# Optimization experiments

Measured on AMD Instinct MI355X. Metric: run time of the kernel, lower is better.

The kernel has to match this reference:

```python
import jax, jax.numpy as jnp
import numpy as np

B, S, D, H, DM = 2, 2048, 1024, 16, 4
HD = D // H  # head_dim = 64
EPS = 1e-5


def setup_inputs() -> dict:
    key = jax.random.key(0)
    ks = jax.random.split(key, 8)
    s = 0.02
    return {
        "x": jax.random.normal(ks[0], (B, S, D), jnp.float32),
        "wq": jax.random.normal(ks[1], (D, D), jnp.float32) * s,
        "wk": jax.random.normal(ks[2], (D, D), jnp.float32) * s,
        "wv": jax.random.normal(ks[3], (D, D), jnp.float32) * s,
        "wo": jax.random.normal(ks[4], (D, D), jnp.float32) * s,
        "bo": jnp.zeros((D,), jnp.float32),
        "ln1_scale": jnp.ones((D,), jnp.float32),
        "ln1_shift": jnp.zeros((D,), jnp.float32),
        "ln2_scale": jnp.ones((D,), jnp.float32),
        "ln2_shift": jnp.zeros((D,), jnp.float32),
        "w1": jax.random.normal(ks[5], (DM * D, D), jnp.float32) * s,
        "b1": jnp.zeros((DM * D,), jnp.float32),
        "w2": jax.random.normal(ks[6], (D, DM * D), jnp.float32) * s,
        "b2": jnp.zeros((D,), jnp.float32),
    }


def _layernorm(x, scale, shift):
    mean = jnp.mean(x, axis=-1, keepdims=True)
    var = jnp.var(x, axis=-1, keepdims=True)  # unbiased=False
    return scale * (x - mean) * jax.lax.rsqrt(var + EPS) + shift


def _attn(x, wq, wk, wv, wo, bo):
    b, n, d = x.shape
    # torch Linear: y = x @ W.T
    q = (x @ wq.T).reshape(b, n, H, HD).transpose(0, 2, 1, 3)  # [b,h,n,hd]
    k = (x @ wk.T).reshape(b, n, H, HD).transpose(0, 2, 1, 3)
    v = (x @ wv.T).reshape(b, n, H, HD).transpose(0, 2, 1, 3)
    scores = jnp.einsum("bhqd,bhkd->bhqk", q, k)
    causal = jnp.tril(jnp.ones((n, n), bool))
    scores = jnp.where(causal, scores, -jnp.inf)
    w = jax.nn.softmax(scores / np.sqrt(HD).astype(np.float32), axis=-1)
    ctx = jnp.einsum("bhqk,bhkd->bhqd", w, v)
    ctx = ctx.transpose(0, 2, 1, 3).reshape(b, n, d)
    return ctx @ wo.T + bo


def reference(x, wq, wk, wv, wo, bo, ln1_scale, ln1_shift, ln2_scale, ln2_shift, w1, b1, w2, b2):
    h = x + _attn(_layernorm(x, ln1_scale, ln1_shift), wq, wk, wv, wo, bo)
    y = _layernorm(h, ln2_scale, ln2_shift)
    y = jax.nn.relu(y @ w1.T + b1) @ w2.T + b2
    return h + y
```

## Files before the change

kernel.cpp:

```cpp
#include <hip/hip_runtime.h>
#include <hip/hip_bf16.h>

#define DEV __device__ __forceinline__

typedef __attribute__((ext_vector_type(8))) short bf8;
typedef __attribute__((ext_vector_type(4))) float f4;
typedef __attribute__((ext_vector_type(16))) float f16x;

DEV unsigned short f2bf(float f) {
  union { __hip_bfloat16 h; unsigned short u; } c;
  c.h = __float2bfloat16(f);
  return c.u;
}
DEV unsigned int pk2(float a, float b) {
  union { __hip_bfloat162 h; unsigned int u; } c;
  c.h = __hip_bfloat162(__float2bfloat16(a), __float2bfloat16(b));
  return c.u;
}

DEV int2 swz_tile(int ob, int nxt, int nyt) {
  const int nb = nxt * nyt;
  const int cpx = nb >> 3;
  const int W = (ob & 7) * cpx + (ob >> 3);
  const int scw = 4 * nyt;
  const int sc = W / scw, rem = W - sc * scw;
  return make_int2(rem >> 2, sc * 4 + (rem & 3));
}

template<bool BIAS, bool RELU, bool OUTBF, bool WRVT>
__global__ __launch_bounds__(512, 2) void gemm_bt256(
    const unsigned short* __restrict__ A, const unsigned short* __restrict__ B,
    const float* __restrict__ bias, void* __restrict__ Cout,
    int M, int N, int K, int ldc, unsigned short* __restrict__ vtout, int nyt)
{
  __shared__ unsigned short Sl[2][2][256 * 64];
  const int t = threadIdx.x;
  const int w = t >> 6, l = t & 63;
  const int wr = w >> 2, wc = w & 3;
  int2 tt = swz_tile((int)blockIdx.x, N >> 8, nyt);
  const int m0 = tt.x * 256, n0 = tt.y * 256;

  const int srow = w * 32 + (l >> 3);
  const int scol = 8 * ((l & 7) ^ (l >> 3));
  const unsigned short* Ab = A + (size_t)(m0 + srow) * K + scol;
  const unsigned short* Bb = B + (size_t)(n0 + srow) * K + scol;
  const int sdst = w * 2048 + l * 8;

  auto STAGE = [&](int slot, int kt) {
#pragma unroll
    for (int i = 0; i < 4; ++i) {
      __builtin_amdgcn_global_load_lds(
          (const __attribute__((address_space(1))) void*)(Ab + (size_t)i * 8 * K + kt * 64),
          (__attribute__((address_space(3))) void*)(&Sl[slot][0][sdst + i * 512]), 16, 0, 0);
      __builtin_amdgcn_global_load_lds(
          (const __attribute__((address_space(1))) void*)(Bb + (size_t)i * 8 * K + kt * 64),
          (__attribute__((address_space(3))) void*)(&Sl[slot][1][sdst + i * 512]), 16, 0, 0);
    }
  };

  const f4 fz = {0.f, 0.f, 0.f, 0.f};
  f4 acc[8][4];
#pragma unroll
  for (int i = 0; i < 8; ++i)
#pragma unroll
    for (int j = 0; j < 4; ++j) acc[i][j] = fz;

  const int NT = K >> 6;
  STAGE(0, 0);
  __syncthreads();

  for (int T = 0; T < NT; ++T) {
    if (T + 1 < NT) STAGE((T + 1) & 1, T + 1);
    const int sl = T & 1;
#pragma unroll
    for (int ks = 0; ks < 2; ++ks) {
      const int cb = (ks * 64 + ((l >> 4) * 16)) ^ ((l & 7) << 4);
      bf8 af[8], bg[4];
#pragma unroll
      for (int m = 0; m < 8; ++m)
        af[m] = *(const bf8*)((const char*)&Sl[sl][0][(wr * 128 + m * 16 + (l & 15)) * 64] + cb);
#pragma unroll
      for (int n = 0; n < 4; ++n)
        bg[n] = *(const bf8*)((const char*)&Sl[sl][1][(wc * 64 + n * 16 + (l & 15)) * 64] + cb);
      __builtin_amdgcn_s_setprio(1);
#pragma unroll
      for (int m = 0; m < 8; ++m)
#pragma unroll
        for (int n = 0; n < 4; ++n)
          acc[m][n] = __builtin_amdgcn_mfma_f32_16x16x32_bf16(af[m], bg[n], acc[m][n], 0, 0, 0);
      __builtin_amdgcn_s_setprio(0);
    }
    __syncthreads();
  }

#pragma unroll
  for (int n = 0; n < 4; ++n) {
    const int col = n0 + wc * 64 + n * 16 + (l & 15);
    float bv = 0.f;
    if (BIAS) bv = bias[col];
    const bool isv = WRVT && (col >= 2048);
    const int hh = (col - 2048) >> 6, dd = (col - 2048) & 63;
#pragma unroll
    for (int m = 0; m < 8; ++m) {
#pragma unroll
      for (int r = 0; r < 4; ++r) {
        const int row = m0 + wr * 128 + m * 16 + ((l >> 4) * 4) + r;
        float v = acc[m][n][r] + bv;
        if (RELU) v = fmaxf(v, 0.f);
        if (WRVT && isv) {
          const int bb = row >> 11, ss = row & 2047;
          vtout[((size_t)(bb * 16 + hh) * 64 + dd) * 2048 + ss] = f2bf(v);
        } else if (OUTBF) {
          ((unsigned short*)Cout)[(size_t)row * ldc + col] = f2bf(v);
        } else {
          ((float*)Cout)[(size_t)row * ldc + col] = v;
        }
      }
    }
  }
}

template<bool BIAS, bool RELU, bool RESID, bool OUTBF>
__global__ __launch_bounds__(256) void gemm_bt(
    const unsigned short* __restrict__ A, const unsigned short* __restrict__ B,
    const float* __restrict__ bias, const float* __restrict__ resid,
    void* __restrict__ Cout, int M, int N, int K, int ldc, int nyt)
{
  __shared__ unsigned short Al[2][128 * 32];
  __shared__ unsigned short Bl[2][128 * 32];
  const int t = threadIdx.x;
  const int w = t >> 6, l = t & 63;
  const int wr = w >> 1, wc = w & 1;
  int2 tt = swz_tile((int)blockIdx.x, N >> 7, nyt);
  const int m0 = tt.x * 128, n0 = tt.y * 128;

  const int srow = w * 16 + (l >> 2);
  const int scsw = ((l & 3) * 8) ^ (((srow >> 1) & 3) << 3);
  const unsigned short* Ab = A + (size_t)(m0 + srow) * K + scsw;
  const unsigned short* Bb = B + (size_t)(n0 + srow) * K + scsw;
  const int sdst = w * 512 + l * 8;

  auto STAGE = [&](int slot, int k0) {
#pragma unroll
    for (int i = 0; i < 2; ++i) {
      __builtin_amdgcn_global_load_lds(
          (const __attribute__((address_space(1))) void*)(Ab + (size_t)i * 64 * K + k0),
          (__attribute__((address_space(3))) void*)(&Al[slot][sdst + i * 2048]), 16, 0, 0);
      __builtin_amdgcn_global_load_lds(
          (const __attribute__((address_space(1))) void*)(Bb + (size_t)i * 64 * K + k0),
          (__attribute__((address_space(3))) void*)(&Bl[slot][sdst + i * 2048]), 16, 0, 0);
    }
  };

  const f4 fz = {0.f, 0.f, 0.f, 0.f};
  f4 acc[4][4];
#pragma unroll
  for (int i = 0; i < 4; ++i)
#pragma unroll
    for (int j = 0; j < 4; ++j) acc[i][j] = fz;

  const int NT = K >> 5;
  STAGE(0, 0);
  __syncthreads();

  for (int T = 0; T < NT; ++T) {
    if (T + 1 < NT) STAGE((T + 1) & 1, (T + 1) * 32);
    const int sl = T & 1;
    const int rdcol = ((l >> 4) * 8) ^ ((((l & 15) >> 1) & 3) << 3);
    bf8 af[4], bg[4];
#pragma unroll
    for (int am = 0; am < 4; ++am)
      af[am] = *(const bf8*)&Al[sl][(wr * 64 + am * 16 + (l & 15)) * 32 + rdcol];
#pragma unroll
    for (int bn = 0; bn < 4; ++bn)
      bg[bn] = *(const bf8*)&Bl[sl][(wc * 64 + bn * 16 + (l & 15)) * 32 + rdcol];
    __builtin_amdgcn_s_setprio(1);
#pragma unroll
    for (int am = 0; am < 4; ++am)
#pragma unroll
      for (int bn = 0; bn < 4; ++bn)
        acc[am][bn] = __builtin_amdgcn_mfma_f32_16x16x32_bf16(af[am], bg[bn], acc[am][bn], 0, 0, 0);
    __builtin_amdgcn_s_setprio(0);
    __syncthreads();
  }

#pragma unroll
  for (int bn = 0; bn < 4; ++bn) {
    const int col = n0 + wc * 64 + bn * 16 + (l & 15);
    float bv = 0.f;
    if (BIAS) bv = bias[col];
#pragma unroll
    for (int am = 0; am < 4; ++am) {
#pragma unroll
      for (int r = 0; r < 4; ++r) {
        const int row = m0 + wr * 64 + am * 16 + ((l >> 4) * 4) + r;
        float v = acc[am][bn][r] + bv;
        if (RELU) v = fmaxf(v, 0.f);
        if (RESID) v += resid[(size_t)row * ldc + col];
        if (OUTBF) ((unsigned short*)Cout)[(size_t)row * ldc + col] = f2bf(v);
        else       ((float*)Cout)[(size_t)row * ldc + col] = v;
      }
    }
  }
}

__global__ __launch_bounds__(128) void attn_kernel(
    const unsigned short* __restrict__ qk, const unsigned short* __restrict__ vt,
    unsigned short* __restrict__ ctx)
{
  __shared__ unsigned short Ks[2][64 * 64];
  __shared__ unsigned short Vs[2][64 * 64];

  const int t = threadIdx.x;
  const int w = t >> 6, l = t & 63;
  const int hi = l >> 5, q = l & 31;
  const int bid = blockIdx.x;
  const int xcd = bid & 7, i = bid >> 3;
  const int g = i >> 5, c = i & 31;
  const int a = (g & 1) ? c : 31 - c;
  const int bh = xcd * 4 + g;
  const int b = bh >> 4, h = bh & 15;
  const int tile = 2 * a + w;
  const int q0w = tile * 32;
  const int nit = a + 1;

  const unsigned short* qbase = qk + ((size_t)b * 2048) * 2048 + h * 64;
  const unsigned short* kbase = qbase + 1024;
  const unsigned short* vbase = vt + (size_t)bh * 64 * 2048;

  bf8 qf[4];
#pragma unroll
  for (int ksl = 0; ksl < 4; ++ksl)
    qf[ksl] = *(const bf8*)(qbase + (size_t)(q0w + q) * 2048 + ksl * 16 + hi * 8);

  f16x oacc[2];
#pragma unroll
  for (int dn = 0; dn < 2; ++dn)
#pragma unroll
    for (int i2 = 0; i2 < 16; ++i2) oacc[dn][i2] = 0.f;
  float m_ = -1e30f, l_ = 0.f;

  auto STAGE = [&](int buf, int it) {
#pragma unroll
    for (int s = 0; s < 4; ++s) {
      const int row = s * 16 + (t >> 3);
      const int cb = (t & 7) * 16;
      const int sb = cb ^ ((row & 7) << 4);
      __builtin_amdgcn_global_load_lds(
          (const __attribute__((address_space(1))) void*)
              (kbase + (size_t)(it * 64 + row) * 2048 + (sb >> 1)),
          (__attribute__((address_space(3))) void*)(&Ks[buf][row * 64 + (cb >> 1)]),
          16, 0, 0);
      __builtin_amdgcn_global_load_lds(
          (const __attribute__((address_space(1))) void*)
              (vbase + (size_t)row * 2048 + it * 64 + (sb >> 1)),
          (__attribute__((address_space(3))) void*)(&Vs[buf][row * 64 + (cb >> 1)]),
          16, 0, 0);
    }
  };

  STAGE(0, 0);
  __syncthreads();

  for (int it = 0; it < nit; ++it) {
    const int buf = it & 1;
    if (it + 1 < nit) STAGE(buf ^ 1, it + 1);
    const int kb0 = it * 64;

    f16x s0, s1;
#pragma unroll
    for (int i2 = 0; i2 < 16; ++i2) { s0[i2] = 0.f; s1[i2] = 0.f; }
    __builtin_amdgcn_s_setprio(1);
#pragma unroll
    for (int ksl = 0; ksl < 4; ++ksl) {
      const int cbq = (ksl * 16 + hi * 8) * 2;
      const int r0 = q, r1 = 32 + q;
      bf8 k0 = *(const bf8*)((const char*)&Ks[buf][r0 * 64] + (cbq ^ ((r0 & 7) << 4)));
      bf8 k1 = *(const bf8*)((const char*)&Ks[buf][r1 * 64] + (cbq ^ ((r1 & 7) << 4)));
      s0 = __builtin_amdgcn_mfma_f32_32x32x16_bf16(k0, qf[ksl], s0, 0, 0, 0);
      s1 = __builtin_amdgcn_mfma_f32_32x32x16_bf16(k1, qf[ksl], s1, 0, 0, 0);
    }
    __builtin_amdgcn_s_setprio(0);

    float p[32];
    if (it == nit - 1) {
#pragma unroll
      for (int i2 = 0; i2 < 16; ++i2) {
        const int key = kb0 + (i2 & 3) + 8 * (i2 >> 2) + 4 * hi;
        p[i2]      = (key <= q0w + q)      ? s0[i2] : -1e30f;
        p[16 + i2] = (key + 32 <= q0w + q) ? s1[i2] : -1e30f;
      }
    } else {
#pragma unroll
      for (int i2 = 0; i2 < 16; ++i2) { p[i2] = s0[i2]; p[16 + i2] = s1[i2]; }
    }

    float tm[16];
#pragma unroll
    for (int i2 = 0; i2 < 16; ++i2) tm[i2] = fmaxf(p[i2], p[16 + i2]);
#pragma unroll
    for (int st = 8; st >= 1; st >>= 1)
#pragma unroll
      for (int i2 = 0; i2 < 8; ++i2)
        if (i2 < st) tm[i2] = fmaxf(tm[i2], tm[i2 + st]);
    const float pmax = fmaxf(tm[0], __shfl_xor(tm[0], 32));
    if (__any(pmax > m_ + 11.54f)) {
      const float mn = fmaxf(m_, pmax);
      const float alpha = __builtin_amdgcn_exp2f(m_ - mn);
      m_ = mn;
      l_ *= alpha;
#pragma unroll
      for (int dn = 0; dn < 2; ++dn)
#pragma unroll
        for (int i2 = 0; i2 < 16; ++i2) oacc[dn][i2] *= alpha;
    }
#pragma unroll
    for (int i2 = 0; i2 < 32; ++i2) p[i2] = __builtin_amdgcn_exp2f(p[i2] - m_);
    float ts[16];
#pragma unroll
    for (int i2 = 0; i2 < 16; ++i2) ts[i2] = p[i2] + p[16 + i2];
#pragma unroll
    for (int st = 8; st >= 1; st >>= 1)
#pragma unroll
      for (int i2 = 0; i2 < 8; ++i2)
        if (i2 < st) ts[i2] += ts[i2 + st];
    l_ += ts[0] + __shfl_xor(ts[0], 32);

#pragma unroll
    for (int sg = 0; sg < 2; ++sg) {
      const float* pp = p + sg * 16;
      unsigned int wds[8];
#pragma unroll
      for (int m = 0; m < 4; ++m) {
        wds[m * 2]     = pk2(pp[4 * m], pp[4 * m + 1]);
        wds[m * 2 + 1] = pk2(pp[4 * m + 2], pp[4 * m + 3]);
      }
#pragma unroll
      for (int kq = 0; kq < 2; ++kq) {
        unsigned int x0 = __shfl_xor((int)(hi ? wds[4 * kq]     : wds[4 * kq + 2]), 32);
        unsigned int x1 = __shfl_xor((int)(hi ? wds[4 * kq + 1] : wds[4 * kq + 3]), 32);
        union { unsigned int u[4]; bf8 v; } pu;
        pu.u[0] = hi ? x0 : wds[4 * kq];
        pu.u[1] = hi ? x1 : wds[4 * kq + 1];
        pu.u[2] = hi ? wds[4 * kq + 2] : x0;
        pu.u[3] = hi ? wds[4 * kq + 3] : x1;
        const bf8 pf = pu.v;
        __builtin_amdgcn_s_setprio(1);
#pragma unroll
        for (int dn = 0; dn < 2; ++dn) {
          const int row = dn * 32 + q;
          const int cb = ((sg * 32 + kq * 16 + hi * 8) * 2) ^ ((row & 7) << 4);
          bf8 vf = *(const bf8*)((const char*)&Vs[buf][row * 64] + cb);
          oacc[dn] = __builtin_amdgcn_mfma_f32_32x32x16_bf16(vf, pf, oacc[dn], 0, 0, 0);
        }
        __builtin_amdgcn_s_setprio(0);
      }
    }
    __syncthreads();
  }

  const float inv = 1.0f / l_;
  unsigned short* crow = ctx + ((size_t)(b * 2048 + q0w + q)) * 1024 + h * 64;
#pragma unroll
  for (int dn = 0; dn < 2; ++dn)
#pragma unroll
    for (int m = 0; m < 4; ++m) {
      const int d0 = dn * 32 + 8 * m + 4 * hi;
      *(unsigned int*)(crow + d0)     = pk2(oacc[dn][4 * m] * inv, oacc[dn][4 * m + 1] * inv);
      *(unsigned int*)(crow + d0 + 2) = pk2(oacc[dn][4 * m + 2] * inv, oacc[dn][4 * m + 3] * inv);
    }
}

__global__ __launch_bounds__(256) void ln_kernel(
    const float* __restrict__ x, const float* __restrict__ sc,
    const float* __restrict__ sh, unsigned short* __restrict__ out)
{
  const int row = blockIdx.x, t = threadIdx.x;
  float4 v = ((const float4*)x)[(size_t)row * 256 + t];
  float s = v.x + v.y + v.z + v.w;
  float q = v.x * v.x + v.y * v.y + v.z * v.z + v.w * v.w;
#pragma unroll
  for (int off = 1; off < 64; off <<= 1) {
    s += __shfl_xor(s, off);
    q += __shfl_xor(q, off);
  }
  __shared__ float red[8];
  const int w = t >> 6, l = t & 63;
  if (l == 0) { red[w] = s; red[4 + w] = q; }
  __syncthreads();
  s = red[0] + red[1] + red[2] + red[3];
  q = red[4] + red[5] + red[6] + red[7];
  const float mean = s * (1.0f / 1024.0f);
  const float var = q * (1.0f / 1024.0f) - mean * mean;
  const float rstd = rsqrtf(var + 1e-5f);
  float4 scv = ((const float4*)sc)[t];
  float4 shv = ((const float4*)sh)[t];
  uint2 p;
  p.x = pk2(scv.x * (v.x - mean) * rstd + shv.x, scv.y * (v.y - mean) * rstd + shv.y);
  p.y = pk2(scv.z * (v.z - mean) * rstd + shv.z, scv.w * (v.w - mean) * rstd + shv.w);
  ((uint2*)out)[(size_t)row * 256 + t] = p;
}

__global__ __launch_bounds__(256) void cvt_weights(
    const float* __restrict__ wq, const float* __restrict__ wk,
    const float* __restrict__ wv, const float* __restrict__ wo,
    const float* __restrict__ w1, const float* __restrict__ w2,
    unsigned short* __restrict__ dst)
{
  const int M1 = 1 << 20;
  const int n4 = (12 * M1) / 4;
  const int stride = gridDim.x * 256;
  for (int i4 = blockIdx.x * 256 + threadIdx.x; i4 < n4; i4 += stride) {
    const size_t i = (size_t)i4 * 4;
    const int mi = (int)(i >> 20);
    const float* src;
    size_t off;
    float sc = 1.0f;
    if (mi < 4) {
      src = mi == 0 ? wq : mi == 1 ? wk : mi == 2 ? wv : wo;
      off = i & (size_t)(M1 - 1);
      if (mi == 0) sc = 0.125f * 1.44269504088896f;
    } else if (mi < 8) {
      src = w1; off = i - (size_t)4 * M1;
    } else {
      src = w2; off = i - (size_t)8 * M1;
    }
    float4 v = *(const float4*)(src + off);
    uint2 pq;
    pq.x = pk2(v.x * sc, v.y * sc);
    pq.y = pk2(v.z * sc, v.w * sc);
    ((uint2*)dst)[i4] = pq;
  }
}

extern "C" void kernel_launch(void* const* d_in, const int* in_sizes, int n_in,
                              void* d_out, int out_size, void* d_ws, size_t ws_size,
                              hipStream_t stream)
{
  const float* x    = (const float*)d_in[0];
  const float* wq   = (const float*)d_in[1];
  const float* wk   = (const float*)d_in[2];
  const float* wv   = (const float*)d_in[3];
  const float* wo   = (const float*)d_in[4];
  const float* bo   = (const float*)d_in[5];
  const float* ln1s = (const float*)d_in[6];
  const float* ln1b = (const float*)d_in[7];
  const float* ln2s = (const float*)d_in[8];
  const float* ln2b = (const float*)d_in[9];
  const float* w1   = (const float*)d_in[10];
  const float* b1   = (const float*)d_in[11];
  const float* w2   = (const float*)d_in[12];
  const float* b2   = (const float*)d_in[13];
  float* out = (float*)d_out;

  const int M = 4096;

  unsigned short* ws   = (unsigned short*)d_ws;
  unsigned short* lnb  = ws;
  unsigned short* qkvw = lnb  + (size_t)4096 * 1024;
  unsigned short* wob  = qkvw + (size_t)3072 * 1024;
  unsigned short* w1b  = wob  + (size_t)1024 * 1024;
  unsigned short* w2b  = w1b  + (size_t)4096 * 1024;
  unsigned short* qkb  = w2b  + (size_t)4096 * 1024;
  unsigned short* vtb  = qkb  + (size_t)4096 * 2048;
  unsigned short* ctxb = vtb  + (size_t)32 * 64 * 2048;
  float* hf = (float*)(ctxb + (size_t)4096 * 1024);

  cvt_weights<<<2048, 256, 0, stream>>>(wq, wk, wv, wo, w1, w2, qkvw);

  ln_kernel<<<M, 256, 0, stream>>>(x, ln1s, ln1b, lnb);
  gemm_bt256<false, false, true, true><<<192, 512, 0, stream>>>(
      lnb, qkvw, nullptr, qkb, M, 3072, 1024, 2048, vtb, 16);
  attn_kernel<<<1024, 128, 0, stream>>>(qkb, vtb, ctxb);
  gemm_bt<true, false, true, false><<<256, 256, 0, stream>>>(
      ctxb, wob, bo, x, hf, M, 1024, 1024, 1024, 32);
  ln_kernel<<<M, 256, 0, stream>>>(hf, ln2s, ln2b, lnb);
  gemm_bt256<true, true, true, false><<<256, 512, 0, stream>>>(
      lnb, w1b, b1, qkb, M, 4096, 1024, 4096, nullptr, 16);
  gemm_bt<true, false, true, false><<<256, 256, 0, stream>>>(
      qkb, w2b, b2, hf, out, M, 1024, 4096, 1024, 32);
}
```

Baseline: 269.5 us.

## Split attention KV range across two wave pairs and merge partial softmax

Doubles the attention block to 256 threads so two pairs of waves each process half of the causal key blocks for the same query tiles, then merge their running max, sum and output accumulators through shared memory (split-K flash attention). This aims to shorten the per-block serial KV loop and improve occupancy and load balance. In exchange it drops the double-buffered prefetch in favour of single-buffered loads with two barriers per iteration, adds a reduction step through LDS, and leaves one pair idle on odd block counts.

```diff
diff --git a/kernel.cpp b/kernel.cpp
--- a/kernel.cpp
+++ b/kernel.cpp
@@ -204,29 +204,32 @@
   }
 }
 
-__global__ __launch_bounds__(128) void attn_kernel(
+__global__ __launch_bounds__(256, 4) void attn_kernel(
     const unsigned short* __restrict__ qk, const unsigned short* __restrict__ vt,
     unsigned short* __restrict__ ctx)
 {
-  __shared__ unsigned short Ks[2][64 * 64];
-  __shared__ unsigned short Vs[2][64 * 64];
+  __shared__ unsigned short SM[2][2][64 * 64];
 
   const int t = threadIdx.x;
   const int w = t >> 6, l = t & 63;
+  const int p = w >> 1;
   const int hi = l >> 5, q = l & 31;
   const int bid = blockIdx.x;
   const int xcd = bid & 7, i = bid >> 3;
   const int g = i >> 5, c = i & 31;
-  const int a = (g & 1) ? c : 31 - c;
+  const int s = (g & 1) ? c : 31 - c;
   const int bh = xcd * 4 + g;
   const int b = bh >> 4, h = bh & 15;
-  const int tile = 2 * a + w;
+  const int tile = 2 * s + (w & 1);
   const int q0w = tile * 32;
-  const int nit = a + 1;
+  const int h0 = (s + 2) >> 1;
 
   const unsigned short* qbase = qk + ((size_t)b * 2048) * 2048 + h * 64;
   const unsigned short* kbase = qbase + 1024;
   const unsigned short* vbase = vt + (size_t)bh * 64 * 2048;
+  unsigned short* Kl = &SM[p][0][0];
+  unsigned short* Vl = &SM[p][1][0];
+  const int tp = t & 127;
 
   bf8 qf[4];
 #pragma unroll
@@ -240,135 +243,158 @@
     for (int i2 = 0; i2 < 16; ++i2) oacc[dn][i2] = 0.f;
   float m_ = -1e30f, l_ = 0.f;
 
-  auto STAGE = [&](int buf, int it) {
-#pragma unroll
-    for (int s = 0; s < 4; ++s) {
-      const int row = s * 16 + (t >> 3);
-      const int cb = (t & 7) * 16;
-      const int sb = cb ^ ((row & 7) << 4);
-      __builtin_amdgcn_global_load_lds(
-          (const __attribute__((address_space(1))) void*)
-              (kbase + (size_t)(it * 64 + row) * 2048 + (sb >> 1)),
-          (__attribute__((address_space(3))) void*)(&Ks[buf][row * 64 + (cb >> 1)]),
-          16, 0, 0);
-      __builtin_amdgcn_global_load_lds(
-          (const __attribute__((address_space(1))) void*)
-              (vbase + (size_t)row * 2048 + it * 64 + (sb >> 1)),
-          (__attribute__((address_space(3))) void*)(&Vs[buf][row * 64 + (cb >> 1)]),
-          16, 0, 0);
-    }
-  };
-
-  STAGE(0, 0);
+  for (int it = 0; it < h0; ++it) {
+    const int gi = p ? h0 + it : it;
+    const bool act = gi <= s;
+    __syncthreads();
+    if (act) {
+#pragma unroll
+      for (int ss = 0; ss < 4; ++ss) {
+        const int row = ss * 16 + (tp >> 3);
+        const int cb = (tp & 7) * 16;
+        const int sb = cb ^ ((row & 7) << 4);
+        __builtin_amdgcn_global_load_lds(
+            (const __attribute__((address_space(1))) void*)
+                (kbase + (size_t)(gi * 64 + row) * 2048 + (sb >> 1)),
+            (__attribute__((address_space(3))) void*)(&Kl[row * 64 + (cb >> 1)]),
+            16, 0, 0);
+        __builtin_amdgcn_global_load_lds(
+            (const __attribute__((address_space(1))) void*)
+                (vbase + (size_t)row * 2048 + gi * 64 + (sb >> 1)),
+            (__attribute__((address_space(3))) void*)(&Vl[row * 64 + (cb >> 1)]),
+            16, 0, 0);
+      }
+    }
+    __syncthreads();
+    if (act) {
+      const int kb0 = gi * 64;
+
+      f16x s0, s1;
+#pragma unroll
+      for (int i2 = 0; i2 < 16; ++i2) { s0[i2] = 0.f; s1[i2] = 0.f; }
+      __builtin_amdgcn_s_setprio(1);
+#pragma unroll
+      for (int ksl = 0; ksl < 4; ++ksl) {
+        const int cbq = (ksl * 16 + hi * 8) * 2;
+        const int r0 = q, r1 = 32 + q;
+        bf8 k0 = *(const bf8*)((const char*)&Kl[r0 * 64] + (cbq ^ ((r0 & 7) << 4)));
+        bf8 k1 = *(const bf8*)((const char*)&Kl[r1 * 64] + (cbq ^ ((r1 & 7) << 4)));
+        s0 = __builtin_amdgcn_mfma_f32_32x32x16_bf16(k0, qf[ksl], s0, 0, 0, 0);
+        s1 = __builtin_amdgcn_mfma_f32_32x32x16_bf16(k1, qf[ksl], s1, 0, 0, 0);
+      }
+      __builtin_amdgcn_s_setprio(0);
+
+      float pv[32];
+      if (gi == s) {
+#pragma unroll
+        for (int i2 = 0; i2 < 16; ++i2) {
+          const int key = kb0 + (i2 & 3) + 8 * (i2 >> 2) + 4 * hi;
+          pv[i2]      = (key <= q0w + q)      ? s0[i2] : -1e30f;
+          pv[16 + i2] = (key + 32 <= q0w + q) ? s1[i2] : -1e30f;
+        }
+      } else {
+#pragma unroll
+        for (int i2 = 0; i2 < 16; ++i2) { pv[i2] = s0[i2]; pv[16 + i2] = s1[i2]; }
+      }
+
+      float tm[16];
+#pragma unroll
+      for (int i2 = 0; i2 < 16; ++i2) tm[i2] = fmaxf(pv[i2], pv[16 + i2]);
+#pragma unroll
+      for (int st = 8; st >= 1; st >>= 1)
+#pragma unroll
+        for (int i2 = 0; i2 < 8; ++i2)
+          if (i2 < st) tm[i2] = fmaxf(tm[i2], tm[i2 + st]);
+      const float pmax = fmaxf(tm[0], __shfl_xor(tm[0], 32));
+      if (__any(pmax > m_ + 11.54f)) {
+        const float mn = fmaxf(m_, pmax);
+        const float alpha = __builtin_amdgcn_exp2f(m_ - mn);
+        m_ = mn;
+        l_ *= alpha;
+#pragma unroll
+        for (int dn = 0; dn < 2; ++dn)
+#pragma unroll
+          for (int i2 = 0; i2 < 16; ++i2) oacc[dn][i2] *= alpha;
+      }
+#pragma unroll
+      for (int i2 = 0; i2 < 32; ++i2) pv[i2] = __builtin_amdgcn_exp2f(pv[i2] - m_);
+      float ts[16];
+#pragma unroll
+      for (int i2 = 0; i2 < 16; ++i2) ts[i2] = pv[i2] + pv[16 + i2];
+#pragma unroll
+      for (int st = 8; st >= 1; st >>= 1)
+#pragma unroll
+        for (int i2 = 0; i2 < 8; ++i2)
+          if (i2 < st) ts[i2] += ts[i2 + st];
+      l_ += ts[0] + __shfl_xor(ts[0], 32);
+
+#pragma unroll
+      for (int sg = 0; sg < 2; ++sg) {
+        const float* pp = pv + sg * 16;
+        unsigned int wds[8];
+#pragma unroll
+        for (int m = 0; m < 4; ++m) {
+          wds[m * 2]     = pk2(pp[4 * m], pp[4 * m + 1]);
+          wds[m * 2 + 1] = pk2(pp[4 * m + 2], pp[4 * m + 3]);
+        }
+#pragma unroll
+        for (int kq = 0; kq < 2; ++kq) {
+          unsigned int x0 = __shfl_xor((int)(hi ? wds[4 * kq]     : wds[4 * kq + 2]), 32);
+          unsigned int x1 = __shfl_xor((int)(hi ? wds[4 * kq + 1] : wds[4 * kq + 3]), 32);
+          union { unsigned int u[4]; bf8 v; } pu;
+          pu.u[0] = hi ? x0 : wds[4 * kq];
+          pu.u[1] = hi ? x1 : wds[4 * kq + 1];
+          pu.u[2] = hi ? wds[4 * kq + 2] : x0;
+          pu.u[3] = hi ? wds[4 * kq + 3] : x1;
+          const bf8 pf = pu.v;
+          __builtin_amdgcn_s_setprio(1);
+#pragma unroll
+          for (int dn = 0; dn < 2; ++dn) {
+            const int row = dn * 32 + q;
+            const int cb = ((sg * 32 + kq * 16 + hi * 8) * 2) ^ ((row & 7) << 4);
+            bf8 vf = *(const bf8*)((const char*)&Vl[row * 64] + cb);
+            oacc[dn] = __builtin_amdgcn_mfma_f32_32x32x16_bf16(vf, pf, oacc[dn], 0, 0, 0);
+          }
+          __builtin_amdgcn_s_setprio(0);
+        }
+      }
+    }
+  }
+
   __syncthreads();
-
-  for (int it = 0; it < nit; ++it) {
-    const int buf = it & 1;
-    if (it + 1 < nit) STAGE(buf ^ 1, it + 1);
-    const int kb0 = it * 64;
-
-    f16x s0, s1;
-#pragma unroll
-    for (int i2 = 0; i2 < 16; ++i2) { s0[i2] = 0.f; s1[i2] = 0.f; }
-    __builtin_amdgcn_s_setprio(1);
-#pragma unroll
-    for (int ksl = 0; ksl < 4; ++ksl) {
-      const int cbq = (ksl * 16 + hi * 8) * 2;
-      const int r0 = q, r1 = 32 + q;
-      bf8 k0 = *(const bf8*)((const char*)&Ks[buf][r0 * 64] + (cbq ^ ((r0 & 7) << 4)));
-      bf8 k1 = *(const bf8*)((const char*)&Ks[buf][r1 * 64] + (cbq ^ ((r1 & 7) << 4)));
-      s0 = __builtin_amdgcn_mfma_f32_32x32x16_bf16(k0, qf[ksl], s0, 0, 0, 0);
-      s1 = __builtin_amdgcn_mfma_f32_32x32x16_bf16(k1, qf[ksl], s1, 0, 0, 0);
-    }
-    __builtin_amdgcn_s_setprio(0);
-
-    float p[32];
-    if (it == nit - 1) {
-#pragma unroll
-      for (int i2 = 0; i2 < 16; ++i2) {
-        const int key = kb0 + (i2 & 3) + 8 * (i2 >> 2) + 4 * hi;
-        p[i2]      = (key <= q0w + q)      ? s0[i2] : -1e30f;
-        p[16 + i2] = (key + 32 <= q0w + q) ? s1[i2] : -1e30f;
-      }
-    } else {
-#pragma unroll
-      for (int i2 = 0; i2 < 16; ++i2) { p[i2] = s0[i2]; p[16 + i2] = s1[i2]; }
-    }
-
-    float tm[16];
-#pragma unroll
-    for (int i2 = 0; i2 < 16; ++i2) tm[i2] = fmaxf(p[i2], p[16 + i2]);
-#pragma unroll
-    for (int st = 8; st >= 1; st >>= 1)
-#pragma unroll
-      for (int i2 = 0; i2 < 8; ++i2)
-        if (i2 < st) tm[i2] = fmaxf(tm[i2], tm[i2 + st]);
-    const float pmax = fmaxf(tm[0], __shfl_xor(tm[0], 32));
-    if (__any(pmax > m_ + 11.54f)) {
-      const float mn = fmaxf(m_, pmax);
-      const float alpha = __builtin_amdgcn_exp2f(m_ - mn);
-      m_ = mn;
-      l_ *= alpha;
-#pragma unroll
-      for (int dn = 0; dn < 2; ++dn)
-#pragma unroll
-        for (int i2 = 0; i2 < 16; ++i2) oacc[dn][i2] *= alpha;
-    }
-#pragma unroll
-    for (int i2 = 0; i2 < 32; ++i2) p[i2] = __builtin_amdgcn_exp2f(p[i2] - m_);
-    float ts[16];
-#pragma unroll
-    for (int i2 = 0; i2 < 16; ++i2) ts[i2] = p[i2] + p[16 + i2];
-#pragma unroll
-    for (int st = 8; st >= 1; st >>= 1)
-#pragma unroll
-      for (int i2 = 0; i2 < 8; ++i2)
-        if (i2 < st) ts[i2] += ts[i2 + st];
-    l_ += ts[0] + __shfl_xor(ts[0], 32);
-
-#pragma unroll
-    for (int sg = 0; sg < 2; ++sg) {
-      const float* pp = p + sg * 16;
-      unsigned int wds[8];
+  float* mb = (float*)&SM[0][0][0];
+  if (p == 1) {
+    float* base = mb + (w & 1) * 2176;
+    base[l] = m_;
+    base[64 + l] = l_;
+#pragma unroll
+    for (int dn = 0; dn < 2; ++dn)
+#pragma unroll
+      for (int i2 = 0; i2 < 16; ++i2)
+        base[128 + (dn * 16 + i2) * 64 + l] = oacc[dn][i2];
+  }
+  __syncthreads();
+  if (p == 0) {
+    float* base = mb + (w & 1) * 2176;
+    const float m2 = base[l], l2 = base[64 + l];
+    const float mm = fmaxf(m_, m2);
+    const float a0 = __builtin_amdgcn_exp2f(m_ - mm);
+    const float a2 = __builtin_amdgcn_exp2f(m2 - mm);
+    const float inv = 1.0f / (a0 * l_ + a2 * l2);
+    unsigned short* crow = ctx + ((size_t)(b * 2048 + q0w + q)) * 1024 + h * 64;
+#pragma unroll
+    for (int dn = 0; dn < 2; ++dn)
 #pragma unroll
       for (int m = 0; m < 4; ++m) {
-        wds[m * 2]     = pk2(pp[4 * m], pp[4 * m + 1]);
-        wds[m * 2 + 1] = pk2(pp[4 * m + 2], pp[4 * m + 3]);
-      }
-#pragma unroll
-      for (int kq = 0; kq < 2; ++kq) {
-        unsigned int x0 = __shfl_xor((int)(hi ? wds[4 * kq]     : wds[4 * kq + 2]), 32);
-        unsigned int x1 = __shfl_xor((int)(hi ? wds[4 * kq + 1] : wds[4 * kq + 3]), 32);
-        union { unsigned int u[4]; bf8 v; } pu;
-        pu.u[0] = hi ? x0 : wds[4 * kq];
-        pu.u[1] = hi ? x1 : wds[4 * kq + 1];
-        pu.u[2] = hi ? wds[4 * kq + 2] : x0;
-        pu.u[3] = hi ? wds[4 * kq + 3] : x1;
-        const bf8 pf = pu.v;
-        __builtin_amdgcn_s_setprio(1);
-#pragma unroll
-        for (int dn = 0; dn < 2; ++dn) {
-          const int row = dn * 32 + q;
-          const int cb = ((sg * 32 + kq * 16 + hi * 8) * 2) ^ ((row & 7) << 4);
-          bf8 vf = *(const bf8*)((const char*)&Vs[buf][row * 64] + cb);
-          oacc[dn] = __builtin_amdgcn_mfma_f32_32x32x16_bf16(vf, pf, oacc[dn], 0, 0, 0);
-        }
-        __builtin_amdgcn_s_setprio(0);
-      }
-    }
-    __syncthreads();
-  }
-
-  const float inv = 1.0f / l_;
-  unsigned short* crow = ctx + ((size_t)(b * 2048 + q0w + q)) * 1024 + h * 64;
-#pragma unroll
-  for (int dn = 0; dn < 2; ++dn)
-#pragma unroll
-    for (int m = 0; m < 4; ++m) {
-      const int d0 = dn * 32 + 8 * m + 4 * hi;
-      *(unsigned int*)(crow + d0)     = pk2(oacc[dn][4 * m] * inv, oacc[dn][4 * m + 1] * inv);
-      *(unsigned int*)(crow + d0 + 2) = pk2(oacc[dn][4 * m + 2] * inv, oacc[dn][4 * m + 3] * inv);
-    }
+        float o0 = a0 * oacc[dn][4 * m]     + a2 * base[128 + (dn * 16 + 4 * m) * 64 + l];
+        float o1 = a0 * oacc[dn][4 * m + 1] + a2 * base[128 + (dn * 16 + 4 * m + 1) * 64 + l];
+        float o2 = a0 * oacc[dn][4 * m + 2] + a2 * base[128 + (dn * 16 + 4 * m + 2) * 64 + l];
+        float o3 = a0 * oacc[dn][4 * m + 3] + a2 * base[128 + (dn * 16 + 4 * m + 3) * 64 + l];
+        const int d0 = dn * 32 + 8 * m + 4 * hi;
+        *(unsigned int*)(crow + d0)     = pk2(o0 * inv, o1 * inv);
+        *(unsigned int*)(crow + d0 + 2) = pk2(o2 * inv, o3 * inv);
+      }
+  }
 }
 
 __global__ __launch_bounds__(256) void ln_kernel(
@@ -471,7 +497,7 @@
   ln_kernel<<<M, 256, 0, stream>>>(x, ln1s, ln1b, lnb);
   gemm_bt256<false, false, true, true><<<192, 512, 0, stream>>>(
       lnb, qkvw, nullptr, qkb, M, 3072, 1024, 2048, vtb, 16);
-  attn_kernel<<<1024, 128, 0, stream>>>(qkb, vtb, ctxb);
+  attn_kernel<<<1024, 256, 0, stream>>>(qkb, vtb, ctxb);
   gemm_bt<true, false, true, false><<<256, 256, 0, stream>>>(
       ctxb, wob, bo, x, hf, M, 1024, 1024, 1024, 32);
   ln_kernel<<<M, 256, 0, stream>>>(hf, ln2s, ln2b, lnb);
```

After: 245.6 us. -8.8%, faster.
